# Kernel optimization log

Measured on AMD Instinct MI355X. Metric: run time of the kernel, lower is better.

The kernel has to match this reference:

```python
import jax, jax.numpy as jnp
import numpy as np

D = 128   # num_variables
H = 16    # hidden_dim
B = 8192  # batch size


def setup_inputs() -> dict:
    key = jax.random.key(0)
    ks = jax.random.split(key, 8)
    X = jax.random.normal(ks[0], (B, D), dtype=jnp.float32)
    adjacency_logits = jax.random.normal(ks[1], (D, D), dtype=jnp.float32) * 0.1
    temperature = jnp.array(1.0, dtype=jnp.float32)
    # Fixed Gumbel noise for F.gumbel_softmax (deterministic reference)
    u = jax.random.uniform(ks[2], (D, D, 2), dtype=jnp.float32, minval=1e-6, maxval=1.0 - 1e-6)
    gumbel = -jnp.log(-jnp.log(u))
    # Stacked per-variable MLP params (torch Linear default init: U(-1/sqrt(fan_in), 1/sqrt(fan_in)))
    lim1 = 1.0 / np.sqrt(D)
    lim2 = 1.0 / np.sqrt(H)
    W1 = jax.random.uniform(ks[3], (D, D, H), dtype=jnp.float32, minval=-lim1, maxval=lim1)  # [var, in, hid]
    b1 = jax.random.uniform(ks[4], (D, H), dtype=jnp.float32, minval=-lim1, maxval=lim1)
    W2 = jax.random.uniform(ks[5], (D, H), dtype=jnp.float32, minval=-lim2, maxval=lim2)     # [var, hid] (out dim 1)
    b2 = jax.random.uniform(ks[6], (D,), dtype=jnp.float32, minval=-lim2, maxval=lim2)
    return {"X": X, "adjacency_logits": adjacency_logits, "temperature": temperature,
            "gumbel": gumbel, "W1": W1, "b1": b1, "W2": W2, "b2": b2}


def _soft_adjacency(adjacency_logits, temperature, gumbel):
    # binary gumbel-softmax over {off, on}, take P(on), zero the diagonal
    logits2 = jnp.stack([-adjacency_logits, adjacency_logits], axis=-1)  # [D, D, 2]
    y = jax.nn.softmax((logits2 + gumbel) / temperature, axis=-1)
    A = y[..., 1] * (1.0 - jnp.eye(adjacency_logits.shape[0], dtype=adjacency_logits.dtype))
    return A


def reference(X, adjacency_logits, temperature, gumbel, W1, b1, W2, b2):
    A = _soft_adjacency(adjacency_logits, temperature, gumbel)  # [D, D], A[v, i] = edge v->i
    # masked input for variable i: X * A[:, i]  ->  masked[b, i, v] = X[b, v] * A[v, i]
    masked = X[:, None, :] * A.T[None, :, :]                    # [B, D, D]
    hidden = jax.nn.relu(jnp.einsum('biv,ivh->bih', masked, W1) + b1)  # [B, D, H]
    recon = jnp.einsum('bih,ih->bi', hidden, W2) + b2            # [B, D]
    return recon, A
```

## Files before the change

### kernel.cpp

```cpp
#include <hip/hip_runtime.h>
#include <hip/hip_fp16.h>

#define DD 128
#define HH 16
#define BB 8192

typedef _Float16 half8 __attribute__((ext_vector_type(8)));
typedef _Float16 half4 __attribute__((ext_vector_type(4)));
typedef float f32x4 __attribute__((ext_vector_type(4)));

__global__ void k_prep(const float* __restrict__ L, const float* __restrict__ Tptr,
                       const float* __restrict__ g, const float* __restrict__ W1,
                       float* __restrict__ Aout, _Float16* __restrict__ Wt) {
    int idx = blockIdx.x * blockDim.x + threadIdx.x;
    int v = idx & (DD - 1);
    int h = (idx >> 7) & (HH - 1);
    int i = idx >> 11;
    int vi = v * DD + i;
    float t = Tptr[0];
    float z = (2.0f * L[vi] + g[2 * vi + 1] - g[2 * vi]) / t;
    float a = 1.0f / (1.0f + __expf(-z));
    if (v == i) a = 0.0f;
    if (h == 0) Aout[vi] = a;
    Wt[idx] = (_Float16)(a * W1[(i * DD + v) * HH + h]);
}

__launch_bounds__(256)
__global__ void k_main(const float* __restrict__ X, const _Float16* __restrict__ Wt,
                       const float* __restrict__ b1, const float* __restrict__ W2,
                       const float* __restrict__ b2, float* __restrict__ out) {
    const int tid  = threadIdx.x;
    const int wave = tid >> 6;
    const int lane = tid & 63;
    const int m    = lane & 15;
    const int q    = lane >> 4;

    const int b0 = blockIdx.x * 128 + wave * 32;
    const int i0 = blockIdx.y * 16;

    half8 xb[2][4];
#pragma unroll
    for (int t = 0; t < 2; t++) {
        const float* xp = X + (b0 + t * 16 + m) * DD + q * 8;
#pragma unroll
        for (int s = 0; s < 4; s++) {
            f32x4 lo = *(const f32x4*)(xp + s * 32);
            f32x4 hi = *(const f32x4*)(xp + s * 32 + 4);
            half8 hf;
            hf[0] = (_Float16)lo[0]; hf[1] = (_Float16)lo[1];
            hf[2] = (_Float16)lo[2]; hf[3] = (_Float16)lo[3];
            hf[4] = (_Float16)hi[0]; hf[5] = (_Float16)hi[1];
            hf[6] = (_Float16)hi[2]; hf[7] = (_Float16)hi[3];
            xb[t][s] = hf;
        }
    }

    f32x4 w2f = *(const f32x4*)(W2 + (i0 + m) * HH + q * 4);
    half4 w2self;
    w2self[0] = (_Float16)w2f[0]; w2self[1] = (_Float16)w2f[1];
    w2self[2] = (_Float16)w2f[2]; w2self[3] = (_Float16)w2f[3];
    const half4 hzero = {(_Float16)0.f, (_Float16)0.f, (_Float16)0.f, (_Float16)0.f};

    const float b2v = b2[i0 + m];
    f32x4 acc2[2];
    acc2[0] = (f32x4){b2v, b2v, b2v, b2v};
    acc2[1] = (f32x4){b2v, b2v, b2v, b2v};

    for (int ii = 0; ii < 16; ii++) {
        const int i = i0 + ii;
        const _Float16* wp = Wt + (i * HH + m) * DD + q * 8;
        f32x4 a0 = {0.f, 0.f, 0.f, 0.f};
        f32x4 a1 = {0.f, 0.f, 0.f, 0.f};
#pragma unroll
        for (int s = 0; s < 4; s++) {
            half8 wa = *(const half8*)(wp + s * 32);
            a0 = __builtin_amdgcn_mfma_f32_16x16x32_f16(wa, xb[0][s], a0, 0, 0, 0);
            a1 = __builtin_amdgcn_mfma_f32_16x16x32_f16(wa, xb[1][s], a1, 0, 0, 0);
        }
        f32x4 b1v = *(const f32x4*)(b1 + i * HH + q * 4);
        half4 p0, p1;
#pragma unroll
        for (int r = 0; r < 4; r++) {
            float t0 = a0[r] + b1v[r];
            float t1 = a1[r] + b1v[r];
            p0[r] = (_Float16)(t0 > 0.f ? t0 : 0.f);
            p1[r] = (_Float16)(t1 > 0.f ? t1 : 0.f);
        }
        half4 bfrag = (m == ii) ? w2self : hzero;
        acc2[0] = __builtin_amdgcn_mfma_f32_16x16x16f16(p0, bfrag, acc2[0], 0, 0, 0);
        acc2[1] = __builtin_amdgcn_mfma_f32_16x16x16f16(p1, bfrag, acc2[1], 0, 0, 0);
    }

#pragma unroll
    for (int t = 0; t < 2; t++)
#pragma unroll
        for (int r = 0; r < 4; r++)
            out[(size_t)(b0 + t * 16 + q * 4 + r) * DD + i0 + m] = acc2[t][r];
}

extern "C" void kernel_launch(void* const* d_in, const int* in_sizes, int n_in,
                              void* d_out, int out_size, void* d_ws, size_t ws_size,
                              hipStream_t stream) {
    const float* X  = (const float*)d_in[0];
    const float* L  = (const float*)d_in[1];
    const float* T  = (const float*)d_in[2];
    const float* g  = (const float*)d_in[3];
    const float* W1 = (const float*)d_in[4];
    const float* b1 = (const float*)d_in[5];
    const float* W2 = (const float*)d_in[6];
    const float* b2 = (const float*)d_in[7];

    float* recon = (float*)d_out;
    float* Aout  = recon + (size_t)BB * DD;

    _Float16* Wt = (_Float16*)d_ws;

    k_prep<<<(DD * HH * DD) / 256, 256, 0, stream>>>(L, T, g, W1, Aout, Wt);

    dim3 grid(BB / 128, DD / 16);
    k_main<<<grid, 256, 0, stream>>>(X, Wt, b1, W2, b2, recon);
}
```

Baseline: 93.19 us.

## Process 64 batch rows per wave to reuse weight fragments across four MFMAs

```diff
diff --git a/kernel.cpp b/kernel.cpp
--- a/kernel.cpp
+++ b/kernel.cpp
@@ -5,9 +5,14 @@
 #define HH 16
 #define BB 8192
 
-typedef _Float16 half8 __attribute__((ext_vector_type(8)));
-typedef _Float16 half4 __attribute__((ext_vector_type(4)));
+typedef _Float16 hf8 __attribute__((ext_vector_type(8)));
+typedef _Float16 hf4 __attribute__((ext_vector_type(4)));
+typedef _Float16 hf2 __attribute__((ext_vector_type(2)));
 typedef float f32x4 __attribute__((ext_vector_type(4)));
+
+static __device__ __forceinline__ hf2 pkrtz(float a, float b) {
+    return __builtin_bit_cast(hf2, __builtin_amdgcn_cvt_pkrtz(a, b));
+}
 
 __global__ void k_prep(const float* __restrict__ L, const float* __restrict__ Tptr,
                        const float* __restrict__ g, const float* __restrict__ W1,
@@ -25,7 +30,7 @@
     Wt[idx] = (_Float16)(a * W1[(i * DD + v) * HH + h]);
 }
 
-__launch_bounds__(256)
+__launch_bounds__(128)
 __global__ void k_main(const float* __restrict__ X, const _Float16* __restrict__ Wt,
                        const float* __restrict__ b1, const float* __restrict__ W2,
                        const float* __restrict__ b2, float* __restrict__ out) {
@@ -35,64 +40,65 @@
     const int m    = lane & 15;
     const int q    = lane >> 4;
 
-    const int b0 = blockIdx.x * 128 + wave * 32;
+    const int b0 = blockIdx.x * 128 + wave * 64;
     const int i0 = blockIdx.y * 16;
 
-    half8 xb[2][4];
+    hf8 xb[4][4];
 #pragma unroll
-    for (int t = 0; t < 2; t++) {
-        const float* xp = X + (b0 + t * 16 + m) * DD + q * 8;
+    for (int t = 0; t < 4; t++) {
+        const float* xp = X + (size_t)(b0 + t * 16 + m) * DD + q * 8;
 #pragma unroll
         for (int s = 0; s < 4; s++) {
             f32x4 lo = *(const f32x4*)(xp + s * 32);
             f32x4 hi = *(const f32x4*)(xp + s * 32 + 4);
-            half8 hf;
-            hf[0] = (_Float16)lo[0]; hf[1] = (_Float16)lo[1];
-            hf[2] = (_Float16)lo[2]; hf[3] = (_Float16)lo[3];
-            hf[4] = (_Float16)hi[0]; hf[5] = (_Float16)hi[1];
-            hf[6] = (_Float16)hi[2]; hf[7] = (_Float16)hi[3];
-            xb[t][s] = hf;
+            hf2 p0 = pkrtz(lo[0], lo[1]);
+            hf2 p1 = pkrtz(lo[2], lo[3]);
+            hf2 p2 = pkrtz(hi[0], hi[1]);
+            hf2 p3 = pkrtz(hi[2], hi[3]);
+            hf4 l4 = __builtin_shufflevector(p0, p1, 0, 1, 2, 3);
+            hf4 h4 = __builtin_shufflevector(p2, p3, 0, 1, 2, 3);
+            xb[t][s] = __builtin_shufflevector(l4, h4, 0, 1, 2, 3, 4, 5, 6, 7);
         }
     }
 
     f32x4 w2f = *(const f32x4*)(W2 + (i0 + m) * HH + q * 4);
-    half4 w2self;
-    w2self[0] = (_Float16)w2f[0]; w2self[1] = (_Float16)w2f[1];
-    w2self[2] = (_Float16)w2f[2]; w2self[3] = (_Float16)w2f[3];
-    const half4 hzero = {(_Float16)0.f, (_Float16)0.f, (_Float16)0.f, (_Float16)0.f};
+    hf2 wlo = pkrtz(w2f[0], w2f[1]);
+    hf2 whi = pkrtz(w2f[2], w2f[3]);
+    hf4 w2self = __builtin_shufflevector(wlo, whi, 0, 1, 2, 3);
+    const hf4 hzero = {(_Float16)0.f, (_Float16)0.f, (_Float16)0.f, (_Float16)0.f};
 
     const float b2v = b2[i0 + m];
-    f32x4 acc2[2];
-    acc2[0] = (f32x4){b2v, b2v, b2v, b2v};
-    acc2[1] = (f32x4){b2v, b2v, b2v, b2v};
+    f32x4 acc2[4];
+#pragma unroll
+    for (int t = 0; t < 4; t++) acc2[t] = (f32x4){b2v, b2v, b2v, b2v};
 
+#pragma unroll 2
     for (int ii = 0; ii < 16; ii++) {
         const int i = i0 + ii;
         const _Float16* wp = Wt + (i * HH + m) * DD + q * 8;
-        f32x4 a0 = {0.f, 0.f, 0.f, 0.f};
-        f32x4 a1 = {0.f, 0.f, 0.f, 0.f};
+        f32x4 b1v = *(const f32x4*)(b1 + i * HH + q * 4);
+        f32x4 a[4] = {b1v, b1v, b1v, b1v};
 #pragma unroll
         for (int s = 0; s < 4; s++) {
-            half8 wa = *(const half8*)(wp + s * 32);
-            a0 = __builtin_amdgcn_mfma_f32_16x16x32_f16(wa, xb[0][s], a0, 0, 0, 0);
-            a1 = __builtin_amdgcn_mfma_f32_16x16x32_f16(wa, xb[1][s], a1, 0, 0, 0);
+            hf8 wa = *(const hf8*)(wp + s * 32);
+#pragma unroll
+            for (int t = 0; t < 4; t++)
+                a[t] = __builtin_amdgcn_mfma_f32_16x16x32_f16(wa, xb[t][s], a[t], 0, 0, 0);
         }
-        f32x4 b1v = *(const f32x4*)(b1 + i * HH + q * 4);
-        half4 p0, p1;
+        hf4 bfrag = (m == ii) ? w2self : hzero;
 #pragma unroll
-        for (int r = 0; r < 4; r++) {
-            float t0 = a0[r] + b1v[r];
-            float t1 = a1[r] + b1v[r];
-            p0[r] = (_Float16)(t0 > 0.f ? t0 : 0.f);
-            p1[r] = (_Float16)(t1 > 0.f ? t1 : 0.f);
+        for (int t = 0; t < 4; t++) {
+            hf2 plo = pkrtz(__builtin_fmaxf(a[t][0], 0.f),
+                            __builtin_fmaxf(a[t][1], 0.f));
+            hf2 phi = pkrtz(__builtin_fmaxf(a[t][2], 0.f),
+                            __builtin_fmaxf(a[t][3], 0.f));
+            hf4 p = __builtin_shufflevector(plo, phi, 0, 1, 2, 3);
+            acc2[t] = __builtin_amdgcn_mfma_f32_16x16x16f16(p, bfrag, acc2[t], 0, 0, 0);
         }
-        half4 bfrag = (m == ii) ? w2self : hzero;
-        acc2[0] = __builtin_amdgcn_mfma_f32_16x16x16f16(p0, bfrag, acc2[0], 0, 0, 0);
-        acc2[1] = __builtin_amdgcn_mfma_f32_16x16x16f16(p1, bfrag, acc2[1], 0, 0, 0);
     }
 
 #pragma unroll
-    for (int t = 0; t < 2; t++)
+    for (int t = 0; t < 4; t++)
 #pragma unroll
         for (int r = 0; r < 4; r++)
             out[(size_t)(b0 + t * 16 + q * 4 + r) * DD + i0 + m] = acc2[t][r];
@@ -118,5 +124,5 @@
     k_prep<<<(DD * HH * DD) / 256, 256, 0, stream>>>(L, T, g, W1, Aout, Wt);
 
     dim3 grid(BB / 128, DD / 16);
-    k_main<<<grid, 256, 0, stream>>>(X, Wt, b1, W2, b2, recon);
+    k_main<<<grid, 128, 0, stream>>>(X, Wt, b1, W2, b2, recon);
 }
```

Measured after the change: 89.49 us. -4.0%, faster.
